# Optimization experiments

Hardware: AMD Instinct MI355X
Metric: run time of the kernel (lower is better)

## Reference

```python
import jax, jax.numpy as jnp
import numpy as np

MODES1 = 16
MODES2 = 16
WIDTH = 64


def spectral_conv2d(x, w):
    # x: [b, ci, n1, n2] real; w: [ci, co, m1, m2, 2] real (re, im)
    b, ci, n1, n2 = x.shape
    co, m1, m2 = w.shape[1], w.shape[2], w.shape[3]
    x_ft = jnp.fft.rfft2(x, norm='ortho')              # [b, ci, n1, n2//2+1] complex
    wc = w[..., 0] + 1j * w[..., 1]                     # [ci, co, m1, m2]
    blk = jnp.einsum('bixy,ioxy->boxy', x_ft[:, :, :m1, :m2], wc)
    out_ft = jnp.zeros((b, co, n1, n2 // 2 + 1), dtype=x_ft.dtype)
    out_ft = out_ft.at[:, :, :m1, :m2].set(blk)
    return jnp.fft.irfft2(out_ft, s=(n1, n2), norm='ortho')


def conv1x1(x, w, bias):
    # x: [b, ci, n1, n2]; w: [co, ci]; bias: [co]
    return jnp.einsum('bixy,oi->boxy', x, w) + bias[None, :, None, None]


def setup_inputs() -> dict:
    key = jax.random.key(0)
    ks = jax.random.split(key, 20)
    B, CIN, N1, N2 = 16, 3, 256, 256
    W = WIDTH
    scale = 1.0 / (W * W)
    inp = {
        'x': jax.random.normal(ks[0], (B, CIN, N1, N2), dtype=jnp.float32),
        'fc0_w': jax.random.normal(ks[1], (W, CIN), dtype=jnp.float32) * 0.1,
        'fc0_b': jnp.zeros((W,), dtype=jnp.float32),
        'sw1': scale * jax.random.normal(ks[2], (W, W, MODES1, MODES2, 2), dtype=jnp.float32),
        'sw2': scale * jax.random.normal(ks[3], (W, W, MODES1, MODES2, 2), dtype=jnp.float32),
        'sw3': scale * jax.random.normal(ks[4], (W, W, MODES1, MODES2, 2), dtype=jnp.float32),
        'sw4': scale * jax.random.normal(ks[5], (W, W, MODES1, MODES2, 2), dtype=jnp.float32),
        'cw1': jax.random.normal(ks[6], (W, W), dtype=jnp.float32) * 0.05,
        'cb1': jnp.zeros((W,), dtype=jnp.float32),
        'cw2': jax.random.normal(ks[7], (W, W), dtype=jnp.float32) * 0.05,
        'cb2': jnp.zeros((W,), dtype=jnp.float32),
        'cw3': jax.random.normal(ks[8], (W, W), dtype=jnp.float32) * 0.05,
        'cb3': jnp.zeros((W,), dtype=jnp.float32),
        'cw4': jax.random.normal(ks[9], (W, W), dtype=jnp.float32) * 0.05,
        'cb4': jnp.zeros((W,), dtype=jnp.float32),
        'fc1_w': jax.random.normal(ks[10], (64, W), dtype=jnp.float32) * 0.05,
        'fc1_b': jnp.zeros((64,), dtype=jnp.float32),
        'fc2_w': jax.random.normal(ks[11], (1, 64), dtype=jnp.float32) * 0.05,
        'fc2_b': jnp.zeros((1,), dtype=jnp.float32),
    }
    return inp


def reference(x, fc0_w, fc0_b, sw1, sw2, sw3, sw4,
              cw1, cb1, cw2, cb2, cw3, cb3, cw4, cb4,
              fc1_w, fc1_b, fc2_w, fc2_b):
    # lift: [b, c, n1, n2] -> channels-last Linear -> [b, width, n1, n2]
    h = jnp.einsum('bcxy,wc->bwxy', x, fc0_w) + fc0_b[None, :, None, None]
    for sw, cw, cb in ((sw1, cw1, cb1), (sw2, cw2, cb2), (sw3, cw3, cb3), (sw4, cw4, cb4)):
        h = jax.nn.gelu(spectral_conv2d(h, sw) + conv1x1(h, cw, cb), approximate=False)
    # projection head (channels-last linears)
    h = jax.nn.gelu(jnp.einsum('bwxy,fw->bfxy', h, fc1_w) + fc1_b[None, :, None, None], approximate=False)
    out = jnp.einsum('bfxy,of->boxy', h, fc2_w) + fc2_b[None, :, None, None]
    return out
```

## Files before the change

### kernel.cpp

```cpp
#include <hip/hip_runtime.h>
#include <math.h>


typedef unsigned int   u32;
typedef unsigned short u16;
typedef __attribute__((ext_vector_type(8))) __bf16 bf16x8;
typedef __attribute__((ext_vector_type(4))) float  f32x4;

constexpr long F1_B  = 134217728;
constexpr long G_B   = 150994944;
constexpr long F2_B  = 167772160;
constexpr long CC_B  = 169869312;
constexpr long WF_B  = 171966464;
constexpr long WXI_B = 171999232;
constexpr long TWF_B = 172032000;
constexpr long BAS_B = 172048384;
constexpr long WSP_B = 172064768;

constexpr int HOP = 76;

union BU { uint2 u2[2]; uint4 u4; bf16x8 v; u16 s[8]; };

__device__ __forceinline__ float gelu_exact(float v) {
    return 0.5f * v * (1.0f + erff(v * 0.70710678118654752440f));
}
__device__ __forceinline__ float bflo(u32 u) { return __uint_as_float(u << 16); }
__device__ __forceinline__ float bfhi(u32 u) { return __uint_as_float(u & 0xffff0000u); }
__device__ __forceinline__ u16 f2bf(float f) {
    u32 u = __float_as_uint(f);
    u += 0x7fffu + ((u >> 16) & 1u);
    return (u16)(u >> 16);
}
__device__ __forceinline__ u32 pack2bf(float a, float b) {
    return (u32)f2bf(a) | ((u32)f2bf(b) << 16);
}

__global__ __launch_bounds__(256) void k_tab(float* __restrict__ wf,
                                             float* __restrict__ wxi,
                                             u16* __restrict__ twf,
                                             u16* __restrict__ bas) {
    const int t = blockIdx.x * 256 + threadIdx.x;
    if (t < 4096) {
        const int y = t >> 4, k = t & 15;
        const int m = (k * y) & 255;
        double s, c; sincospi((double)m / 128.0, &s, &c);
        wf[t * 2] = (float)c; wf[t * 2 + 1] = (float)(-s);
    } else if (t < 8192) {
        const int u = t - 4096;
        const int k1 = u >> 8, x = u & 255;
        const int m = (k1 * x) & 255;
        double s, c; sincospi((double)m / 128.0, &s, &c);
        wxi[u * 2] = (float)c; wxi[u * 2 + 1] = (float)s;
    } else if (t < 16384) {
        const int u = t - 8192;
        const int kc = u >> 8, y = u & 255;
        const int k2 = kc >> 1;
        const int m = (k2 * y) & 255;
        double s, c; sincospi((double)m / 128.0, &s, &c);
        twf[kc * 256 + y] = f2bf((kc & 1) ? (float)(-s) : (float)c);
    } else {
        const int u = t - 16384;
        const int y = u >> 5, kc = u & 31;
        const int k2 = kc >> 1;
        const int m = (k2 * y) & 255;
        double s, c; sincospi((double)m / 128.0, &s, &c);
        const float cc = (k2 == 0) ? 1.0f : 2.0f;
        bas[y * 32 + kc] = f2bf((kc & 1) ? (float)(-cc * s) : (float)(cc * c));
    }
}

__global__ __launch_bounds__(256) void k_wsplit(const float* __restrict__ c1,
                                                const float* __restrict__ c2,
                                                const float* __restrict__ c3,
                                                const float* __restrict__ c4,
                                                const float* __restrict__ f1w,
                                                u16* __restrict__ wsp) {
    const int t = blockIdx.x * 256 + threadIdx.x;
    const int w = t >> 12, p = t & 4095;
    const float* src = (w == 0) ? c1 : (w == 1) ? c2 : (w == 2) ? c3
                     : (w == 3) ? c4 : f1w;
    const float f = src[p];
    const u16 hi = f2bf(f);
    const u16 lo = f2bf(f - __uint_as_float((u32)hi << 16));
    u16* dst = wsp + w * 8192 + (p >> 6) * 128 + (p & 63);
    dst[0]  = hi;
    dst[64] = lo;
}

__device__ __forceinline__ void f1t_epilogue(const u16* HOyo,
                                             const u16* __restrict__ twf,
                                             u16* __restrict__ f1,
                                             int b, int x, int tid) {
    const int lane = tid & 63, wave = tid >> 6;
    const int quad = lane >> 4, col = lane & 15;
    const int o = wave * 16 + col;
    f32x4 a0 = {0.f, 0.f, 0.f, 0.f}, a1 = {0.f, 0.f, 0.f, 0.f};
    #pragma unroll
    for (int ks = 0; ks < 8; ks++) {
        const int kb = ks * 32 + quad * 8;
        BU bb;
        #pragma unroll
        for (int j = 0; j < 8; j++) bb.s[j] = HOyo[(kb + j) * HOP + o];
        const bf16x8 af0 = *(const bf16x8*)(twf + col * 256 + kb);
        const bf16x8 af1 = *(const bf16x8*)(twf + (16 + col) * 256 + kb);
        a0 = __builtin_amdgcn_mfma_f32_16x16x32_bf16(af0, bb.v, a0, 0, 0, 0);
        a1 = __builtin_amdgcn_mfma_f32_16x16x32_bf16(af1, bb.v, a1, 0, 0, 0);
    }
    u16* dst = f1 + (((long)(b * 64 + o)) * 256 + x) * 32 + quad * 4;
    uint2 w;
    w.x = pack2bf(a0[0], a0[1]); w.y = pack2bf(a0[2], a0[3]);
    *(uint2*)dst = w;
    w.x = pack2bf(a1[0], a1[1]); w.y = pack2bf(a1[2], a1[3]);
    *(uint2*)(dst + 16) = w;
}

__global__ __launch_bounds__(256) void k_lift(const float* __restrict__ xin,
                                              const float* __restrict__ w0,
                                              const float* __restrict__ b0,
                                              u16* __restrict__ h,
                                              const u16* __restrict__ twf,
                                              u16* __restrict__ f1) {
    __shared__ float ws0[192], bs0[64];
    __shared__ u16 HOyo[256 * HOP];
    const int tid = threadIdx.x;
    if (tid < 192) ws0[tid] = w0[tid];
    if (tid < 64)  bs0[tid] = b0[tid];
    __syncthreads();
    const int b = blockIdx.x >> 8, x = blockIdx.x & 255;
    const long pix = (((long)b * 3) * 256 + x) * 256 + tid;
    const float x0 = xin[pix];
    const float x1 = xin[pix + 65536];
    const float x2 = xin[pix + 131072];
    u32 pr[32];
    #pragma unroll
    for (int w = 0; w < 64; w += 2) {
        float v0 = bs0[w], v1 = bs0[w + 1];
        v0 = fmaf(x0, ws0[w * 3],     v0);  v1 = fmaf(x0, ws0[w * 3 + 3], v1);
        v0 = fmaf(x1, ws0[w * 3 + 1], v0);  v1 = fmaf(x1, ws0[w * 3 + 4], v1);
        v0 = fmaf(x2, ws0[w * 3 + 2], v0);  v1 = fmaf(x2, ws0[w * 3 + 5], v1);
        pr[w >> 1] = pack2bf(v0, v1);
    }
    u16* hrow = h + (((long)(b * 256 + x)) << 14) + (long)tid * 64;
    #pragma unroll
    for (int q = 0; q < 8; q++) *(uint4*)(hrow + q * 8) = ((uint4*)pr)[q];
    #pragma unroll
    for (int q = 0; q < 16; q++)
        *(uint2*)(HOyo + tid * HOP + q * 4) = ((uint2*)pr)[q];
    __syncthreads();
    f1t_epilogue(HOyo, twf, f1, b, x, tid);
}

__global__ __launch_bounds__(256) void k_dftx(const u16* __restrict__ f1,
                                              const float* __restrict__ wf,
                                              float* __restrict__ f2) {
    const int tid = threadIdx.x;
    const int k1 = tid >> 4, k2 = tid & 15;
    const u16* base = f1 + (long)blockIdx.x * 8192;
    float cr0 = 0, ci0 = 0, cr1 = 0, ci1 = 0;
    for (int x = 0; x < 256; x += 2) {
        const u32 wa = *(const u32*)(base + x * 32 + k2 * 2);
        const float2 ta = *(const float2*)(wf + x * 32 + k1 * 2);
        const float Far = bflo(wa), Fai = bfhi(wa);
        cr0 = fmaf(Far, ta.x, fmaf(-Fai, ta.y, cr0));
        ci0 = fmaf(Fai, ta.x, fmaf(Far, ta.y, ci0));
        const u32 wb = *(const u32*)(base + (x + 1) * 32 + k2 * 2);
        const float2 tb = *(const float2*)(wf + (x + 1) * 32 + k1 * 2);
        const float Fbr = bflo(wb), Fbi = bfhi(wb);
        cr1 = fmaf(Fbr, tb.x, fmaf(-Fbi, tb.y, cr1));
        ci1 = fmaf(Fbi, tb.x, fmaf(Fbr, tb.y, ci1));
    }
    const int m = k1 * 16 + k2;
    *(float2*)(f2 + ((long)m * 1024 + blockIdx.x) * 2) =
        make_float2(cr0 + cr1, ci0 + ci1);
}

__global__ __launch_bounds__(256) void k_mode(const float* __restrict__ f2,
                                              const float* __restrict__ sw,
                                              float* __restrict__ cc) {
    __shared__ __align__(16) float wsh[8192];
    __shared__ __align__(16) float fsh[2048];
    const int tid = threadIdx.x;
    const int m = blockIdx.x;
    const float scale = 1.0f / 65536.0f;
    for (int p = tid; p < 4096; p += 256) {
        const float2 w = *(const float2*)(sw + ((long)p * 256 + m) * 2);
        wsh[p * 2]     = w.x * scale;
        wsh[p * 2 + 1] = w.y * scale;
    }
    for (int t = tid; t < 2048; t += 256) fsh[t] = f2[(long)m * 2048 + t];
    __syncthreads();
    const int b = tid >> 4, o0 = (tid & 15) * 4;
    float re[4] = {0, 0, 0, 0}, im[4] = {0, 0, 0, 0};
    for (int i = 0; i < 64; i++) {
        const float2 F = *(const float2*)(fsh + (b * 64 + i) * 2);
        #pragma unroll
        for (int oo = 0; oo < 4; oo++) {
            const float2 W = *(const float2*)(wsh + (i * 64 + o0 + oo) * 2);
            re[oo] = fmaf(F.x, W.x, fmaf(-F.y, W.y, re[oo]));
            im[oo] = fmaf(F.x, W.y, fmaf(F.y, W.x, im[oo]));
        }
    }
    #pragma unroll
    for (int oo = 0; oo < 4; oo++) {
        *(float2*)(cc + ((long)m * 1024 + b * 64 + o0 + oo) * 2) =
            make_float2(re[oo], im[oo]);
    }
}

__global__ __launch_bounds__(256) void k_invx(const float* __restrict__ cc,
                                              const float* __restrict__ wxi,
                                              u16* __restrict__ g) {
    __shared__ __align__(16) float csh[512];
    const int tid = threadIdx.x;
    const int blk = blockIdx.x;
    const int b = blk >> 6, o = blk & 63;
    ((float2*)csh)[tid] = *(const float2*)(cc + ((long)tid * 1024 + blk) * 2);
    __syncthreads();
    const int x = tid;
    float ar[16], ai[16];
    #pragma unroll
    for (int k = 0; k < 16; k++) { ar[k] = 0; ai[k] = 0; }
    for (int k1 = 0; k1 < 16; k1++) {
        const float2 t = *(const float2*)(wxi + (k1 * 256 + x) * 2);
        #pragma unroll
        for (int k2 = 0; k2 < 16; k2++) {
            const float2 C = ((const float2*)csh)[k1 * 16 + k2];
            ar[k2] = fmaf(C.x, t.x, fmaf(-C.y, t.y, ar[k2]));
            ai[k2] = fmaf(C.x, t.y, fmaf(C.y, t.x, ai[k2]));
        }
    }
    u32 wbuf[16];
    #pragma unroll
    for (int k = 0; k < 16; k++) wbuf[k] = pack2bf(ar[k], ai[k]);
    u16* ob = g + (((long)(b * 256 + x)) * 64 + o) * 32;
    #pragma unroll
    for (int q = 0; q < 4; q++) *(uint4*)(ob + q * 8) = ((uint4*)wbuf)[q];
}

__device__ __forceinline__ void conv_phase1(const u16* __restrict__ h, long hbase,
                                            const u16* __restrict__ Gbf,
                                            const u16* __restrict__ wsp,
                                            const u16* __restrict__ bas,
                                            int b, int x, int tid, f32x4 (*acc)[4]) {
    const int lane = tid & 63, wave = tid >> 6;
    const int quad = lane >> 4, col = lane & 15;
    #pragma unroll
    for (int ks = 0; ks < 2; ks++) {
        bf16x8 B[4], Ah[4], Al[4];
        #pragma unroll
        for (int nt = 0; nt < 4; nt++) {
            const int y = wave * 64 + nt * 16 + col;
            B[nt] = *(const bf16x8*)(h + hbase + (long)y * 64 + ks * 32 + quad * 8);
        }
        #pragma unroll
        for (int mt = 0; mt < 4; mt++) {
            Ah[mt] = *(const bf16x8*)(wsp + (mt * 16 + col) * 128 + ks * 32 + quad * 8);
            Al[mt] = *(const bf16x8*)(wsp + (mt * 16 + col) * 128 + 64 + ks * 32 + quad * 8);
        }
        #pragma unroll
        for (int mt = 0; mt < 4; mt++)
            #pragma unroll
            for (int nt = 0; nt < 4; nt++) {
                acc[mt][nt] = __builtin_amdgcn_mfma_f32_16x16x32_bf16(Ah[mt], B[nt], acc[mt][nt], 0, 0, 0);
                acc[mt][nt] = __builtin_amdgcn_mfma_f32_16x16x32_bf16(Al[mt], B[nt], acc[mt][nt], 0, 0, 0);
            }
    }
    {
        bf16x8 B[4], Ag[4];
        #pragma unroll
        for (int nt = 0; nt < 4; nt++) {
            const int y = wave * 64 + nt * 16 + col;
            B[nt] = *(const bf16x8*)(bas + y * 32 + quad * 8);
        }
        #pragma unroll
        for (int mt = 0; mt < 4; mt++)
            Ag[mt] = *(const bf16x8*)(Gbf + (((long)(b * 256 + x)) * 64 + mt * 16 + col) * 32 + quad * 8);
        #pragma unroll
        for (int mt = 0; mt < 4; mt++)
            #pragma unroll
            for (int nt = 0; nt < 4; nt++)
                acc[mt][nt] = __builtin_amdgcn_mfma_f32_16x16x32_bf16(Ag[mt], B[nt], acc[mt][nt], 0, 0, 0);
    }
}

__global__ __launch_bounds__(256, 4) void k_conv(u16* __restrict__ h,
                                                 const u16* __restrict__ Gbf,
                                                 const u16* __restrict__ wsp,
                                                 const float* __restrict__ cb,
                                                 const u16* __restrict__ bas,
                                                 const u16* __restrict__ twf,
                                                 u16* __restrict__ f1) {
    __shared__ u16 HOyo[256 * HOP];
    const int tid = threadIdx.x;
    const int b = blockIdx.x >> 8, x = blockIdx.x & 255;
    const long hbase = ((long)(b * 256 + x)) << 14;
    f32x4 acc[4][4];
    const f32x4 z = {0.f, 0.f, 0.f, 0.f};
    #pragma unroll
    for (int i = 0; i < 4; i++)
        #pragma unroll
        for (int j = 0; j < 4; j++) acc[i][j] = z;
    conv_phase1(h, hbase, Gbf, wsp, bas, b, x, tid, acc);
    const int lane = tid & 63, wave = tid >> 6;
    const int quad = lane >> 4, col = lane & 15;
    #pragma unroll
    for (int mt = 0; mt < 4; mt++) {
        const int o0 = mt * 16 + quad * 4;
        const float4 cbv = *(const float4*)(cb + o0);
        #pragma unroll
        for (int nt = 0; nt < 4; nt++) {
            const int y = wave * 64 + nt * 16 + col;
            uint2 w;
            w.x = pack2bf(gelu_exact(acc[mt][nt][0] + cbv.x), gelu_exact(acc[mt][nt][1] + cbv.y));
            w.y = pack2bf(gelu_exact(acc[mt][nt][2] + cbv.z), gelu_exact(acc[mt][nt][3] + cbv.w));
            *(uint2*)(HOyo + y * HOP + o0) = w;
        }
    }
    __syncthreads();
    {
        uint2 tmp[16];
        const u16* sr = HOyo + tid * HOP;
        #pragma unroll
        for (int k = 0; k < 16; k++) tmp[k] = *(const uint2*)(sr + k * 4);
        u16* dh = h + hbase + (long)tid * 64;
        #pragma unroll
        for (int q = 0; q < 8; q++) *(uint4*)(dh + q * 8) = ((uint4*)tmp)[q];
    }
    f1t_epilogue(HOyo, twf, f1, b, x, tid);
}

__global__ __launch_bounds__(256, 3) void k_conv_head(const u16* __restrict__ h,
                                                      const u16* __restrict__ Gbf,
                                                      const u16* __restrict__ wsp,
                                                      const float* __restrict__ cb,
                                                      const u16* __restrict__ bas,
                                                      const u16* __restrict__ w1sp,
                                                      const float* __restrict__ b1,
                                                      const float* __restrict__ w2,
                                                      const float* __restrict__ b2,
                                                      float* __restrict__ out) {
    __shared__ u16 HOyo[256 * HOP];
    const int tid = threadIdx.x;
    const int b = blockIdx.x >> 8, x = blockIdx.x & 255;
    const long hbase = ((long)(b * 256 + x)) << 14;
    const float bias2 = b2[0];
    f32x4 acc[4][4];
    const f32x4 z = {0.f, 0.f, 0.f, 0.f};
    #pragma unroll
    for (int i = 0; i < 4; i++)
        #pragma unroll
        for (int j = 0; j < 4; j++) acc[i][j] = z;
    conv_phase1(h, hbase, Gbf, wsp, bas, b, x, tid, acc);
    const int lane = tid & 63, wave = tid >> 6;
    const int quad = lane >> 4, col = lane & 15;
    #pragma unroll
    for (int mt = 0; mt < 4; mt++) {
        const int o0 = mt * 16 + quad * 4;
        const float4 cbv = *(const float4*)(cb + o0);
        #pragma unroll
        for (int nt = 0; nt < 4; nt++) {
            const int y = wave * 64 + nt * 16 + col;
            uint2 w;
            w.x = pack2bf(gelu_exact(acc[mt][nt][0] + cbv.x), gelu_exact(acc[mt][nt][1] + cbv.y));
            w.y = pack2bf(gelu_exact(acc[mt][nt][2] + cbv.z), gelu_exact(acc[mt][nt][3] + cbv.w));
            *(uint2*)(HOyo + y * HOP + o0) = w;
        }
    }
    __syncthreads();
    f32x4 acc2[4][4];
    #pragma unroll
    for (int i = 0; i < 4; i++)
        #pragma unroll
        for (int j = 0; j < 4; j++) acc2[i][j] = z;
    #pragma unroll
    for (int ks = 0; ks < 4; ks++) {
        const int kk = (ks & 1) * 32 + quad * 8;
        bf16x8 B[4], A[4];
        #pragma unroll
        for (int nt = 0; nt < 4; nt++) {
            const int y = wave * 64 + nt * 16 + col;
            BU bb;
            bb.u2[0] = *(const uint2*)(HOyo + y * HOP + kk);
            bb.u2[1] = *(const uint2*)(HOyo + y * HOP + kk + 4);
            B[nt] = bb.v;
        }
        #pragma unroll
        for (int mt = 0; mt < 4; mt++)
            A[mt] = *(const bf16x8*)(w1sp + (mt * 16 + col) * 128 + ks * 32 + quad * 8);
        #pragma unroll
        for (int mt = 0; mt < 4; mt++)
            #pragma unroll
            for (int nt = 0; nt < 4; nt++)
                acc2[mt][nt] = __builtin_amdgcn_mfma_f32_16x16x32_bf16(A[mt], B[nt], acc2[mt][nt], 0, 0, 0);
    }
    float p4[4] = {0.f, 0.f, 0.f, 0.f};
    #pragma unroll
    for (int mt = 0; mt < 4; mt++) {
        const int f0 = mt * 16 + quad * 4;
        const float4 b1v = *(const float4*)(b1 + f0);
        const float4 w2v = *(const float4*)(w2 + f0);
        #pragma unroll
        for (int r = 0; r < 4; r++) {
            const float bb = (&b1v.x)[r];
            const float ww = (&w2v.x)[r];
            #pragma unroll
            for (int nt = 0; nt < 4; nt++)
                p4[nt] = fmaf(ww, gelu_exact(acc2[mt][nt][r] + bb), p4[nt]);
        }
    }
    #pragma unroll
    for (int nt = 0; nt < 4; nt++) {
        p4[nt] += __shfl_xor(p4[nt], 16);
        p4[nt] += __shfl_xor(p4[nt], 32);
    }
    out[(long)b * 65536 + x * 256 + wave * 64 + lane] = p4[quad] + bias2;
}

extern "C" void kernel_launch(void* const* d_in, const int* in_sizes, int n_in,
                              void* d_out, int out_size, void* d_ws, size_t ws_size,
                              hipStream_t stream) {
    const float* x     = (const float*)d_in[0];
    const float* fc0_w = (const float*)d_in[1];
    const float* fc0_b = (const float*)d_in[2];
    const float* sw[4] = {(const float*)d_in[3], (const float*)d_in[4],
                          (const float*)d_in[5], (const float*)d_in[6]};
    const float* cwA[4] = {(const float*)d_in[7],  (const float*)d_in[9],
                           (const float*)d_in[11], (const float*)d_in[13]};
    const float* cbA[4] = {(const float*)d_in[8],  (const float*)d_in[10],
                           (const float*)d_in[12], (const float*)d_in[14]};
    const float* fc1_w = (const float*)d_in[15];
    const float* fc1_b = (const float*)d_in[16];
    const float* fc2_w = (const float*)d_in[17];
    const float* fc2_b = (const float*)d_in[18];

    char* base = (char*)d_ws;
    u16*   h    = (u16*)base;
    u16*   f1   = (u16*)(base + F1_B);
    u16*   Gbf  = (u16*)(base + G_B);
    float* f2   = (float*)(base + F2_B);
    float* cbuf = (float*)(base + CC_B);
    float* wf   = (float*)(base + WF_B);
    float* wxi  = (float*)(base + WXI_B);
    u16*   twf  = (u16*)(base + TWF_B);
    u16*   bas  = (u16*)(base + BAS_B);
    u16*   wsp  = (u16*)(base + WSP_B);

    k_tab<<<96, 256, 0, stream>>>(wf, wxi, twf, bas);
    k_wsplit<<<80, 256, 0, stream>>>(cwA[0], cwA[1], cwA[2], cwA[3], fc1_w, wsp);
    k_lift<<<4096, 256, 0, stream>>>(x, fc0_w, fc0_b, h, twf, f1);
    for (int l = 0; l < 4; l++) {
        k_dftx<<<1024, 256, 0, stream>>>(f1, wf, f2);
        k_mode<<<256, 256, 0, stream>>>(f2, sw[l], cbuf);
        k_invx<<<1024, 256, 0, stream>>>(cbuf, wxi, Gbf);
        if (l < 3) {
            k_conv<<<4096, 256, 0, stream>>>(h, Gbf, wsp + l * 8192, cbA[l],
                                             bas, twf, f1);
        } else {
            k_conv_head<<<4096, 256, 0, stream>>>(h, Gbf, wsp + 3 * 8192, cbA[3],
                                                  bas, wsp + 4 * 8192, fc1_b,
                                                  fc2_w, fc2_b, (float*)d_out);
        }
    }
}
```

Baseline: 1.061 ms.

## Transpose spectral weights, stage DFT input in LDS, approximate GELU, widen invx

Adds a per-layer kernel that transposes and pre-scales the spectral weights into a mode-major layout, so k_mode reads them contiguously instead of with a 256-element stride. k_dftx now stages its f1 block in shared memory before the x loop. k_mode writes its output in a layout that lets k_invx read contiguously, and each k_invx block now handles two output channels with half as many blocks. Exact erf GELU is replaced by the Abramowitz-Stegun polynomial with a hardware reciprocal and a fast exp, which trades a little accuracy for fewer instructions. The transposed weights are kept in the G buffer, which k_invx later overwrites.

```diff
diff --git a/kernel.cpp b/kernel.cpp
--- a/kernel.cpp
+++ b/kernel.cpp
@@ -21,8 +21,17 @@
 
 union BU { uint2 u2[2]; uint4 u4; bf16x8 v; u16 s[8]; };
 
-__device__ __forceinline__ float gelu_exact(float v) {
-    return 0.5f * v * (1.0f + erff(v * 0.70710678118654752440f));
+__device__ __forceinline__ float gelu_fast(float v) {
+    const float ax = fabsf(v) * 0.70710678118654752440f;
+    const float t = __builtin_amdgcn_rcpf(fmaf(0.3275911f, ax, 1.0f));
+    float poly = fmaf(1.061405429f, t, -1.453152027f);
+    poly = fmaf(poly, t, 1.421413741f);
+    poly = fmaf(poly, t, -0.284496736f);
+    poly = fmaf(poly, t, 0.254829592f);
+    poly *= t;
+    const float pe = poly * __expf(-ax * ax);
+    const float w = (v >= 0.0f) ? (2.0f - pe) : pe;
+    return 0.5f * v * w;
 }
 __device__ __forceinline__ float bflo(u32 u) { return __uint_as_float(u << 16); }
 __device__ __forceinline__ float bfhi(u32 u) { return __uint_as_float(u & 0xffff0000u); }
@@ -87,6 +96,27 @@
     dst[64] = lo;
 }
 
+__global__ __launch_bounds__(256) void k_swT(const float* __restrict__ sw,
+                                             float2* __restrict__ swT) {
+    __shared__ float2 tile[64][65];
+    const int tid = threadIdx.x;
+    const int pt = blockIdx.x >> 2, mt = blockIdx.x & 3;
+    const int r = tid >> 2, q = tid & 3;
+    const float scale = 1.0f / 65536.0f;
+    const float2* src = (const float2*)sw + (long)(pt * 64 + r) * 256 + mt * 64 + q * 16;
+    #pragma unroll
+    for (int j = 0; j < 16; j++) {
+        float2 v = src[j];
+        v.x *= scale; v.y *= scale;
+        tile[r][q * 16 + j] = v;
+    }
+    __syncthreads();
+    float2* dst = swT + (long)(mt * 64 + r) * 4096 + pt * 64 + q * 16;
+    #pragma unroll
+    for (int j = 0; j < 16; j++)
+        dst[j] = tile[q * 16 + j][r];
+}
+
 __device__ __forceinline__ void f1t_epilogue(const u16* HOyo,
                                              const u16* __restrict__ twf,
                                              u16* __restrict__ f1,
@@ -153,17 +183,22 @@
 __global__ __launch_bounds__(256) void k_dftx(const u16* __restrict__ f1,
                                               const float* __restrict__ wf,
                                               float* __restrict__ f2) {
-    const int tid = threadIdx.x;
+    __shared__ u32 fsh[4096];
+    const int tid = threadIdx.x;
+    const uint4* src = (const uint4*)(f1 + (long)blockIdx.x * 8192);
+    uint4* dst = (uint4*)fsh;
+    #pragma unroll
+    for (int q = 0; q < 4; q++) dst[q * 256 + tid] = src[q * 256 + tid];
+    __syncthreads();
     const int k1 = tid >> 4, k2 = tid & 15;
-    const u16* base = f1 + (long)blockIdx.x * 8192;
     float cr0 = 0, ci0 = 0, cr1 = 0, ci1 = 0;
     for (int x = 0; x < 256; x += 2) {
-        const u32 wa = *(const u32*)(base + x * 32 + k2 * 2);
+        const u32 wa = fsh[x * 16 + k2];
         const float2 ta = *(const float2*)(wf + x * 32 + k1 * 2);
         const float Far = bflo(wa), Fai = bfhi(wa);
         cr0 = fmaf(Far, ta.x, fmaf(-Fai, ta.y, cr0));
         ci0 = fmaf(Fai, ta.x, fmaf(Far, ta.y, ci0));
-        const u32 wb = *(const u32*)(base + (x + 1) * 32 + k2 * 2);
+        const u32 wb = fsh[(x + 1) * 16 + k2];
         const float2 tb = *(const float2*)(wf + (x + 1) * 32 + k1 * 2);
         const float Fbr = bflo(wb), Fbi = bfhi(wb);
         cr1 = fmaf(Fbr, tb.x, fmaf(-Fbi, tb.y, cr1));
@@ -175,66 +210,66 @@
 }
 
 __global__ __launch_bounds__(256) void k_mode(const float* __restrict__ f2,
-                                              const float* __restrict__ sw,
+                                              const float2* __restrict__ swT,
                                               float* __restrict__ cc) {
-    __shared__ __align__(16) float wsh[8192];
-    __shared__ __align__(16) float fsh[2048];
+    __shared__ float2 wsh[4096];
+    __shared__ float2 fsh[1024];
     const int tid = threadIdx.x;
     const int m = blockIdx.x;
-    const float scale = 1.0f / 65536.0f;
-    for (int p = tid; p < 4096; p += 256) {
-        const float2 w = *(const float2*)(sw + ((long)p * 256 + m) * 2);
-        wsh[p * 2]     = w.x * scale;
-        wsh[p * 2 + 1] = w.y * scale;
-    }
-    for (int t = tid; t < 2048; t += 256) fsh[t] = f2[(long)m * 2048 + t];
+    const float2* wsrc = swT + (long)m * 4096;
+    for (int p = tid; p < 4096; p += 256) wsh[p] = wsrc[p];
+    const float2* fsrc = (const float2*)(f2 + (long)m * 2048);
+    for (int t = tid; t < 1024; t += 256) fsh[t] = fsrc[t];
     __syncthreads();
     const int b = tid >> 4, o0 = (tid & 15) * 4;
     float re[4] = {0, 0, 0, 0}, im[4] = {0, 0, 0, 0};
     for (int i = 0; i < 64; i++) {
-        const float2 F = *(const float2*)(fsh + (b * 64 + i) * 2);
+        const float2 F = fsh[b * 64 + i];
         #pragma unroll
         for (int oo = 0; oo < 4; oo++) {
-            const float2 W = *(const float2*)(wsh + (i * 64 + o0 + oo) * 2);
+            const float2 W = wsh[i * 64 + o0 + oo];
             re[oo] = fmaf(F.x, W.x, fmaf(-F.y, W.y, re[oo]));
             im[oo] = fmaf(F.x, W.y, fmaf(F.y, W.x, im[oo]));
         }
     }
     #pragma unroll
-    for (int oo = 0; oo < 4; oo++) {
-        *(float2*)(cc + ((long)m * 1024 + b * 64 + o0 + oo) * 2) =
+    for (int oo = 0; oo < 4; oo++)
+        *(float2*)(cc + ((long)(b * 64 + o0 + oo) * 256 + m) * 2) =
             make_float2(re[oo], im[oo]);
-    }
 }
 
 __global__ __launch_bounds__(256) void k_invx(const float* __restrict__ cc,
                                               const float* __restrict__ wxi,
                                               u16* __restrict__ g) {
-    __shared__ __align__(16) float csh[512];
-    const int tid = threadIdx.x;
-    const int blk = blockIdx.x;
-    const int b = blk >> 6, o = blk & 63;
-    ((float2*)csh)[tid] = *(const float2*)(cc + ((long)tid * 1024 + blk) * 2);
+    __shared__ float2 csh[2][256];
+    const int tid = threadIdx.x;
+    const int b = blockIdx.x >> 5, o0 = (blockIdx.x & 31) * 2;
+    const float2* src = (const float2*)(cc + ((long)(b * 64 + o0) * 256) * 2);
+    ((float2*)csh)[tid]       = src[tid];
+    ((float2*)csh)[tid + 256] = src[tid + 256];
     __syncthreads();
     const int x = tid;
-    float ar[16], ai[16];
-    #pragma unroll
-    for (int k = 0; k < 16; k++) { ar[k] = 0; ai[k] = 0; }
-    for (int k1 = 0; k1 < 16; k1++) {
-        const float2 t = *(const float2*)(wxi + (k1 * 256 + x) * 2);
-        #pragma unroll
-        for (int k2 = 0; k2 < 16; k2++) {
-            const float2 C = ((const float2*)csh)[k1 * 16 + k2];
-            ar[k2] = fmaf(C.x, t.x, fmaf(-C.y, t.y, ar[k2]));
-            ai[k2] = fmaf(C.x, t.y, fmaf(C.y, t.x, ai[k2]));
-        }
-    }
-    u32 wbuf[16];
-    #pragma unroll
-    for (int k = 0; k < 16; k++) wbuf[k] = pack2bf(ar[k], ai[k]);
-    u16* ob = g + (((long)(b * 256 + x)) * 64 + o) * 32;
-    #pragma unroll
-    for (int q = 0; q < 4; q++) *(uint4*)(ob + q * 8) = ((uint4*)wbuf)[q];
+    u32 wbuf[32];
+    #pragma unroll
+    for (int oo = 0; oo < 2; oo++) {
+        float ar[16], ai[16];
+        #pragma unroll
+        for (int k = 0; k < 16; k++) { ar[k] = 0; ai[k] = 0; }
+        for (int k1 = 0; k1 < 16; k1++) {
+            const float2 t = *(const float2*)(wxi + (k1 * 256 + x) * 2);
+            #pragma unroll
+            for (int k2 = 0; k2 < 16; k2++) {
+                const float2 C = csh[oo][k1 * 16 + k2];
+                ar[k2] = fmaf(C.x, t.x, fmaf(-C.y, t.y, ar[k2]));
+                ai[k2] = fmaf(C.x, t.y, fmaf(C.y, t.x, ai[k2]));
+            }
+        }
+        #pragma unroll
+        for (int k = 0; k < 16; k++) wbuf[oo * 16 + k] = pack2bf(ar[k], ai[k]);
+    }
+    u16* ob = g + ((long)(b * 256 + x) * 64 + o0) * 32;
+    #pragma unroll
+    for (int q = 0; q < 8; q++) *(uint4*)(ob + q * 8) = ((uint4*)wbuf)[q];
 }
 
 __device__ __forceinline__ void conv_phase1(const u16* __restrict__ h, long hbase,
@@ -311,8 +346,8 @@
         for (int nt = 0; nt < 4; nt++) {
             const int y = wave * 64 + nt * 16 + col;
             uint2 w;
-            w.x = pack2bf(gelu_exact(acc[mt][nt][0] + cbv.x), gelu_exact(acc[mt][nt][1] + cbv.y));
-            w.y = pack2bf(gelu_exact(acc[mt][nt][2] + cbv.z), gelu_exact(acc[mt][nt][3] + cbv.w));
+            w.x = pack2bf(gelu_fast(acc[mt][nt][0] + cbv.x), gelu_fast(acc[mt][nt][1] + cbv.y));
+            w.y = pack2bf(gelu_fast(acc[mt][nt][2] + cbv.z), gelu_fast(acc[mt][nt][3] + cbv.w));
             *(uint2*)(HOyo + y * HOP + o0) = w;
         }
     }
@@ -361,8 +396,8 @@
         for (int nt = 0; nt < 4; nt++) {
             const int y = wave * 64 + nt * 16 + col;
             uint2 w;
-            w.x = pack2bf(gelu_exact(acc[mt][nt][0] + cbv.x), gelu_exact(acc[mt][nt][1] + cbv.y));
-            w.y = pack2bf(gelu_exact(acc[mt][nt][2] + cbv.z), gelu_exact(acc[mt][nt][3] + cbv.w));
+            w.x = pack2bf(gelu_fast(acc[mt][nt][0] + cbv.x), gelu_fast(acc[mt][nt][1] + cbv.y));
+            w.y = pack2bf(gelu_fast(acc[mt][nt][2] + cbv.z), gelu_fast(acc[mt][nt][3] + cbv.w));
             *(uint2*)(HOyo + y * HOP + o0) = w;
         }
     }
@@ -405,7 +440,7 @@
             const float ww = (&w2v.x)[r];
             #pragma unroll
             for (int nt = 0; nt < 4; nt++)
-                p4[nt] = fmaf(ww, gelu_exact(acc2[mt][nt][r] + bb), p4[nt]);
+                p4[nt] = fmaf(ww, gelu_fast(acc2[mt][nt][r] + bb), p4[nt]);
         }
     }
     #pragma unroll
@@ -449,9 +484,10 @@
     k_wsplit<<<80, 256, 0, stream>>>(cwA[0], cwA[1], cwA[2], cwA[3], fc1_w, wsp);
     k_lift<<<4096, 256, 0, stream>>>(x, fc0_w, fc0_b, h, twf, f1);
     for (int l = 0; l < 4; l++) {
+        k_swT<<<256, 256, 0, stream>>>(sw[l], (float2*)Gbf);
         k_dftx<<<1024, 256, 0, stream>>>(f1, wf, f2);
-        k_mode<<<256, 256, 0, stream>>>(f2, sw[l], cbuf);
-        k_invx<<<1024, 256, 0, stream>>>(cbuf, wxi, Gbf);
+        k_mode<<<256, 256, 0, stream>>>(f2, (const float2*)Gbf, cbuf);
+        k_invx<<<512, 256, 0, stream>>>(cbuf, wxi, Gbf);
         if (l < 3) {
             k_conv<<<4096, 256, 0, stream>>>(h, Gbf, wsp + l * 8192, cbA[l],
                                              bas, twf, f1);
```

New measurement: 923.8 us. 12.9% less time.
